# Kernel tuning notes

Measured on AMD Instinct MI355X. Metric: run time of the kernel, lower is better.

Reference implementation:

```python
import jax, jax.numpy as jnp
import numpy as np

B, S, E = 2, 1024, 2048
NH = 8          # num attention heads
KVH = 1         # num key/value heads (GQA)
DH = E // NH    # head dim = 256
CAP = 15.0      # gate soft cap
EPS = 1e-6


def setup_inputs() -> dict:
    key = jax.random.key(0)
    ks = jax.random.split(key, 11)
    g = lambda k, shape, sc=0.02: (jax.random.normal(k, shape, jnp.float32) * sc)
    return {
        "x": jax.random.normal(ks[0], (B, S, E), jnp.float32),
        "Wq": g(ks[1], (E, NH * DH)),
        "Wk": g(ks[2], (E, KVH * DH)),
        "Wv": g(ks[3], (E, KVH * DH)),
        "Wog": g(ks[4], (E, E)),
        "Wi": g(ks[5], (E, NH)),
        "bi": g(ks[6], (NH,), 0.1),
        "Wf": g(ks[7], (E, NH)),
        "bf": jnp.ones((NH,), jnp.float32) * 2.0,  # bias forget gate open, as in xLSTM practice
        "gamma": jnp.ones((E,), jnp.float32),       # multihead layernorm weight
        "Wout": g(ks[8], (E, E)),
    }


def _soft_cap(z):
    return CAP * jnp.tanh(z / CAP)


def _repeat_kv(h, n_rep):
    # (B, KVH, S, DH) -> (B, KVH*n_rep, S, DH)
    if n_rep == 1:
        return h
    b, kvh, s, d = h.shape
    return jnp.broadcast_to(h[:, :, None], (b, kvh, n_rep, s, d)).reshape(b, kvh * n_rep, s, d)


def reference(x, Wq, Wk, Wv, Wog, Wi, bi, Wf, bf, gamma, Wout):
    # --- projections ---
    q = (x @ Wq).reshape(B, S, NH, DH).transpose(0, 2, 1, 3)          # (B,NH,S,DH)
    k = (x @ Wk).reshape(B, S, KVH, DH).transpose(0, 2, 1, 3)         # (B,KVH,S,DH)
    v = (x @ Wv).reshape(B, S, KVH, DH).transpose(0, 2, 1, 3)
    k = _repeat_kv(k, NH // KVH)
    v = _repeat_kv(v, NH // KVH)
    o_preact = x @ Wog                                                # (B,S,E)
    i_pre = _soft_cap(x @ Wi + bi).transpose(0, 2, 1)                 # (B,NH,S)
    f_pre = _soft_cap(x @ Wf + bf).transpose(0, 2, 1)                 # (B,NH,S)

    # --- parallel (stabilized) mLSTM backend ---
    logf = jax.nn.log_sigmoid(f_pre)
    cf = jnp.cumsum(logf, axis=-1)                                    # (B,NH,S)
    mat_logf = cf[:, :, :, None] - cf[:, :, None, :]                  # (B,NH,S,S)
    ltr = jnp.tril(jnp.ones((S, S), dtype=bool))
    mat_logD = jnp.where(ltr, mat_logf, -jnp.inf) + i_pre[:, :, None, :]
    vecM = jnp.max(mat_logD, axis=-1, keepdims=True)                  # (B,NH,S,1)
    matD = jnp.exp(mat_logD - vecM)
    matS = jnp.einsum('bhsd,bhtd->bhst', q, k) * (DH ** -0.5)
    matCt = matS * matD
    vecN = jnp.maximum(jnp.abs(matCt.sum(-1, keepdims=True)), jnp.exp(-vecM))
    matC = matCt / (vecN + EPS)
    h = jnp.einsum('bhst,bhtd->bhsd', matC, v)                        # (B,NH,S,DH)

    # --- multihead layernorm (per-head, float32 reductions) ---
    h = h.transpose(0, 2, 1, 3)                                       # (B,S,NH,DH)
    hf = h.astype(jnp.float32)
    mu = hf.mean(-1, keepdims=True)
    var = hf.var(-1, keepdims=True)
    h_norm = ((hf - mu) * jax.lax.rsqrt(var + EPS)).astype(h.dtype)
    h_norm = (h_norm * gamma.reshape(NH, DH)).reshape(B, S, E)

    # --- output gate + projection ---
    y = (jax.nn.sigmoid(o_preact) * h_norm) @ Wout
    return y
```

## Files before the change

### kernel.cpp

```cpp
#include <hip/hip_runtime.h>
#include <math.h>

#define S_LEN  1024
#define EMB    2048
#define NH_    8
#define DH_    256
#define TOKENS 2048
#define NBH    16
#define NQKVO  4736

typedef __attribute__((ext_vector_type(4))) float    f32x4;
typedef __attribute__((ext_vector_type(8))) _Float16 f16x8;
typedef __attribute__((ext_vector_type(4))) _Float16 f16x4;

__device__ __forceinline__ _Float16 f2h(float f) { return (_Float16)f; }

__device__ __forceinline__ void gload16(const void* g, void* l) {
  __builtin_amdgcn_global_load_lds(
      (const __attribute__((address_space(1))) void*)g,
      (__attribute__((address_space(3))) void*)l, 16, 0, 0);
}

__global__ __launch_bounds__(256) void prep_kernel(
    const float* __restrict__ x,
    const float* __restrict__ Wq, const float* __restrict__ Wk,
    const float* __restrict__ Wv, const float* __restrict__ Wog,
    const float* __restrict__ Wout,
    const float* __restrict__ Wi, const float* __restrict__ Wf,
    _Float16* __restrict__ xh,
    _Float16* __restrict__ WcatT, _Float16* __restrict__ WoutT)
{
  __shared__ float shmem[64][65];
  int t = blockIdx.x;
  const int tid = threadIdx.x;
  if (t < TOKENS) {
    const long base = (long)t * EMB + tid * 8;
    const float4 a = *(const float4*)(x + base);
    const float4 b = *(const float4*)(x + base + 4);
    f16x8 o = {f2h(a.x), f2h(a.y), f2h(a.z), f2h(a.w),
               f2h(b.x), f2h(b.y), f2h(b.z), f2h(b.w)};
    *(f16x8*)(xh + base) = o;
  } else if (t < TOKENS + 3328) {
    t -= TOKENS;
    const float* in; _Float16* out; int ldi, ct;
    if (t < 1024)      { in = Wq;   out = WcatT;                    ldi = 2048; ct = 32; }
    else if (t < 1152) { t -= 1024; in = Wk;  out = WcatT + (long)2048 * EMB; ldi = 256; ct = 4; }
    else if (t < 1280) { t -= 1152; in = Wv;  out = WcatT + (long)2304 * EMB; ldi = 256; ct = 4; }
    else if (t < 2304) { t -= 1280; in = Wog; out = WcatT + (long)2560 * EMB; ldi = 2048; ct = 32; }
    else               { t -= 2304; in = Wout; out = WoutT;         ldi = 2048; ct = 32; }
    const long c0 = (long)(t % ct) * 64, r0 = (long)(t / ct) * 64;
    const int lx = tid & 63, ly = tid >> 6;
    #pragma unroll
    for (int i = 0; i < 16; ++i)
      shmem[ly + i * 4][lx] = in[(r0 + ly + i * 4) * ldi + c0 + lx];
    __syncthreads();
    #pragma unroll
    for (int i = 0; i < 16; ++i)
      out[(c0 + ly + i * 4) * EMB + r0 + lx] = f2h(shmem[lx][ly + i * 4]);
  } else {
    const int j = t - (TOKENS + 3328);
    const int row = 4608 + j * 2 + (tid >> 7);
    const int c0 = (tid & 127) * 16;
    _Float16* dst = WcatT + (long)row * EMB + c0;
    if (row < 4616) {
      const int jj = row - 4608;
      #pragma unroll
      for (int k = 0; k < 16; ++k) dst[k] = f2h(Wi[(long)(c0 + k) * 8 + jj]);
    } else if (row < 4624) {
      const int jj = row - 4616;
      #pragma unroll
      for (int k = 0; k < 16; ++k) dst[k] = f2h(Wf[(long)(c0 + k) * 8 + jj]);
    } else {
      #pragma unroll
      for (int k = 0; k < 16; ++k) dst[k] = (_Float16)0.0f;
    }
  }
}

template<typename CT, int BM>
__global__ __launch_bounds__(256) void gemm_bt_kernel(
    const _Float16* __restrict__ Ag, const _Float16* __restrict__ Btg,
    CT* __restrict__ Cg, int K, int lda, int ldb, int ldc, int mtiles)
{
  constexpr int MR = BM / 32;
  __shared__ _Float16 As[3][BM * 32];
  __shared__ _Float16 Bs[3][128 * 32];
  const int tid = threadIdx.x;
  const int lane = tid & 63, wid = tid >> 6;
  const int cpx = gridDim.x >> 3;
  const int wg = ((int)blockIdx.x & 7) * cpx + ((int)blockIdx.x >> 3);
  const int m0 = (wg % mtiles) * BM;
  const int n0 = (wg / mtiles) * 128;
  const _Float16* Ap = Ag + (long)m0 * lda;
  const _Float16* Bp = Btg + (long)n0 * ldb;
  const int wr = wid >> 1, wc = wid & 1;
  const int lrow = lane & 15, kseg = lane >> 4;

  auto stage = [&](int b, int k0) {
    #pragma unroll
    for (int i = 0; i < BM / 64; ++i) {
      const int cbase = (i * 4 + wid) * 64;
      const int row = (cbase >> 2) + (lane >> 2);
      const int src = ((lane & 3) ^ ((row >> 1) & 3)) * 8;
      gload16(Ap + (long)row * lda + k0 + src, (char*)As[b] + cbase * 16);
    }
    #pragma unroll
    for (int i = 0; i < 2; ++i) {
      const int cbase = (i * 4 + wid) * 64;
      const int row = (cbase >> 2) + (lane >> 2);
      const int src = ((lane & 3) ^ ((row >> 1) & 3)) * 8;
      gload16(Bp + (long)row * ldb + k0 + src, (char*)Bs[b] + cbase * 16);
    }
  };

  const int nt = K >> 5;
  f32x4 acc[MR][4] = {};
  stage(0, 0);
  if (nt > 1) stage(1, 32);
  for (int t = 0; t < nt; ++t) {
    if (t + 2 < nt) {
      stage((t + 2) % 3, (t + 2) * 32);
      if constexpr (BM == 128) asm volatile("s_waitcnt vmcnt(8)" ::: "memory");
      else                     asm volatile("s_waitcnt vmcnt(6)" ::: "memory");
    } else if (t + 1 < nt) {
      if constexpr (BM == 128) asm volatile("s_waitcnt vmcnt(4)" ::: "memory");
      else                     asm volatile("s_waitcnt vmcnt(3)" ::: "memory");
    } else {
      asm volatile("s_waitcnt vmcnt(0)" ::: "memory");
    }
    __builtin_amdgcn_s_barrier();
    __builtin_amdgcn_sched_barrier(0);
    const int buf = t % 3;
    f16x8 fa[MR], fb[4];
    #pragma unroll
    for (int m = 0; m < MR; ++m) {
      const int row = wr * (BM / 2) + m * 16 + lrow;
      fa[m] = *(const f16x8*)&As[buf][row * 32 + ((kseg ^ ((row >> 1) & 3)) << 3)];
    }
    #pragma unroll
    for (int n = 0; n < 4; ++n) {
      const int row = wc * 64 + n * 16 + lrow;
      fb[n] = *(const f16x8*)&Bs[buf][row * 32 + ((kseg ^ ((row >> 1) & 3)) << 3)];
    }
    #pragma unroll
    for (int m = 0; m < MR; ++m)
      #pragma unroll
      for (int n = 0; n < 4; ++n)
        acc[m][n] = __builtin_amdgcn_mfma_f32_16x16x32_f16(fa[m], fb[n], acc[m][n], 0, 0, 0);
    __builtin_amdgcn_s_barrier();
  }
  #pragma unroll
  for (int m = 0; m < MR; ++m)
    #pragma unroll
    for (int n = 0; n < 4; ++n)
      #pragma unroll
      for (int i = 0; i < 4; ++i) {
        const int r = m0 + wr * (BM / 2) + m * 16 + kseg * 4 + i;
        const int c = n0 + wc * 64 + n * 16 + lrow;
        Cg[(long)r * ldc + c] = (CT)acc[m][n][i];
      }
}

__global__ __launch_bounds__(256) void gemm_out_kernel(
    const _Float16* __restrict__ Ag, const _Float16* __restrict__ Btg,
    float* __restrict__ Cg, int K, int lda, int ldb, int ldc, int mtiles)
{
  __shared__ _Float16 As[2][64 * 64];
  __shared__ _Float16 Bs[2][128 * 64];
  const int tid = threadIdx.x;
  const int lane = tid & 63, wid = tid >> 6;
  const int cpx = gridDim.x >> 3;
  const int wg = ((int)blockIdx.x & 7) * cpx + ((int)blockIdx.x >> 3);
  const int m0 = (wg % mtiles) * 64;
  const int n0 = (wg / mtiles) * 128;
  const _Float16* Ap = Ag + (long)m0 * lda;
  const _Float16* Bp = Btg + (long)n0 * ldb;
  const int wr = wid >> 1, wc = wid & 1;
  const int lrow = lane & 15, kseg = lane >> 4;

  auto stage = [&](int b, int k0) {
    #pragma unroll
    for (int i = 0; i < 2; ++i) {
      const int cbase = (i * 4 + wid) * 64;
      const int c = cbase + lane;
      const int row = c >> 3, slot = c & 7;
      gload16(Ap + (long)row * lda + k0 + (slot ^ (row & 7)) * 8,
              (char*)As[b] + cbase * 16);
    }
    #pragma unroll
    for (int i = 0; i < 4; ++i) {
      const int cbase = (i * 4 + wid) * 64;
      const int c = cbase + lane;
      const int row = c >> 3, slot = c & 7;
      gload16(Bp + (long)row * ldb + k0 + (slot ^ (row & 7)) * 8,
              (char*)Bs[b] + cbase * 16);
    }
  };

  const int nt = K >> 6;
  f32x4 acc[2][4] = {};
  stage(0, 0);
  int buf = 0;
  for (int t = 0; t < nt; ++t) {
    if (t + 1 < nt) {
      stage(buf ^ 1, (t + 1) * 64);
      asm volatile("s_waitcnt vmcnt(6)" ::: "memory");
    } else {
      asm volatile("s_waitcnt vmcnt(0)" ::: "memory");
    }
    __builtin_amdgcn_s_barrier();
    __builtin_amdgcn_sched_barrier(0);
    #pragma unroll
    for (int kk = 0; kk < 2; ++kk) {
      f16x8 fa[2], fb[4];
      #pragma unroll
      for (int m = 0; m < 2; ++m) {
        const int row = wr * 32 + m * 16 + lrow;
        fa[m] = *(const f16x8*)&As[buf][row * 64 + (((kk * 4 + kseg) ^ (row & 7)) << 3)];
      }
      #pragma unroll
      for (int n = 0; n < 4; ++n) {
        const int row = wc * 64 + n * 16 + lrow;
        fb[n] = *(const f16x8*)&Bs[buf][row * 64 + (((kk * 4 + kseg) ^ (row & 7)) << 3)];
      }
      #pragma unroll
      for (int m = 0; m < 2; ++m)
        #pragma unroll
        for (int n = 0; n < 4; ++n)
          acc[m][n] = __builtin_amdgcn_mfma_f32_16x16x32_f16(fa[m], fb[n], acc[m][n], 0, 0, 0);
    }
    __builtin_amdgcn_s_barrier();
    buf ^= 1;
  }
  #pragma unroll
  for (int m = 0; m < 2; ++m)
    #pragma unroll
    for (int n = 0; n < 4; ++n)
      #pragma unroll
      for (int i = 0; i < 4; ++i) {
        const int r = m0 + wr * 32 + m * 16 + kseg * 4 + i;
        const int c = n0 + wc * 64 + n * 16 + lrow;
        Cg[(long)r * ldc + c] = acc[m][n][i];
      }
}

__global__ __launch_bounds__(256) void mid_kernel(
    const _Float16* __restrict__ qkvo, _Float16* __restrict__ vt,
    const float* __restrict__ bi, const float* __restrict__ bfg,
    float* __restrict__ aArr, float* __restrict__ mArr, float* __restrict__ vMArr)
{
  __shared__ float shmem[64][65];
  const int tid = threadIdx.x;
  int t = blockIdx.x;
  if (t < NBH) {
    const int bh = t;
    const int b = bh >> 3, h = bh & 7;
    const int lane = tid & 63, wid = tid >> 6;
    float* wsum = &shmem[0][0];
    float* wmax = &shmem[1][0];
    const float bih = bi[h], bfh = bfg[h];
    const int s4 = tid * 4;
    const _Float16* zb = qkvo + (long)(b * S_LEN + s4) * NQKVO;
    float zf[4], zi[4];
    #pragma unroll
    for (int k = 0; k < 4; ++k) {
      zi[k] = 15.0f * tanhf(((float)zb[(long)k * NQKVO + 4608 + h] + bih) * (1.0f / 15.0f));
      zf[k] = 15.0f * tanhf(((float)zb[(long)k * NQKVO + 4616 + h] + bfh) * (1.0f / 15.0f));
    }
    float lg[4];
    #pragma unroll
    for (int k = 0; k < 4; ++k)
      lg[k] = fminf(zf[k], 0.0f) - log1pf(expf(-fabsf(zf[k])));
    float c0 = lg[0], c1 = c0 + lg[1], c2 = c1 + lg[2], c3 = c2 + lg[3];
    float ts = c3;
    #pragma unroll
    for (int off = 1; off < 64; off <<= 1) {
      const float o = __shfl_up(ts, off);
      if (lane >= off) ts += o;
    }
    const float texcl = ts - c3;
    if (lane == 63) wsum[wid] = ts;
    __syncthreads();
    float woff = 0.0f;
    for (int w = 0; w < wid; ++w) woff += wsum[w];
    const float base = woff + texcl;
    const float cf[4] = { base + c0, base + c1, base + c2, base + c3 };
    const float a[4] = { zi[0] - cf[0], zi[1] - cf[1], zi[2] - cf[2], zi[3] - cf[3] };
    float l1 = fmaxf(a[0], a[1]), l3 = fmaxf(fmaxf(l1, a[2]), a[3]);
    float incl = l3;
    #pragma unroll
    for (int off = 1; off < 64; off <<= 1) {
      const float o = __shfl_up(incl, off);
      if (lane >= off) incl = fmaxf(incl, o);
    }
    float excl = __shfl_up(incl, 1);
    if (lane == 0) excl = -3.0e38f;
    if (lane == 63) wmax[wid] = incl;
    __syncthreads();
    float wpre = -3.0e38f;
    for (int w = 0; w < wid; ++w) wpre = fmaxf(wpre, wmax[w]);
    const float pre = fmaxf(wpre, excl);
    float mm[4];
    mm[0] = fmaxf(pre, a[0]); mm[1] = fmaxf(mm[0], a[1]);
    mm[2] = fmaxf(mm[1], a[2]); mm[3] = fmaxf(mm[2], a[3]);
    float4 av = { a[0], a[1], a[2], a[3] };
    float4 mv = { mm[0], mm[1], mm[2], mm[3] };
    float4 vv = { cf[0] + mm[0], cf[1] + mm[1], cf[2] + mm[2], cf[3] + mm[3] };
    *(float4*)(aArr + (long)bh * S_LEN + s4) = av;
    *(float4*)(mArr + (long)bh * S_LEN + s4) = mv;
    *(float4*)(vMArr + (long)bh * S_LEN + s4) = vv;
  } else {
    t -= NBH;
    const int z = t >> 6, rem = t & 63;
    const long c0 = (long)(rem & 3) * 64;
    const long r0 = (long)(rem >> 2) * 64;
    const _Float16* ipt = qkvo + (long)z * S_LEN * NQKVO + 2304;
    _Float16* op = vt + (long)z * DH_ * S_LEN;
    const int lx = tid & 63, ly = tid >> 6;
    #pragma unroll
    for (int i = 0; i < 16; ++i)
      shmem[ly + i * 4][lx] = (float)ipt[(r0 + ly + i * 4) * NQKVO + c0 + lx];
    __syncthreads();
    #pragma unroll
    for (int i = 0; i < 16; ++i)
      op[(c0 + ly + i * 4) * S_LEN + r0 + lx] = f2h(shmem[lx][ly + i * 4]);
  }
}

__global__ __launch_bounds__(512) void att_fused_kernel(
    const _Float16* __restrict__ qkvo, const _Float16* __restrict__ vt,
    const float* __restrict__ aArr, const float* __restrict__ mArr,
    const float* __restrict__ vMArr, const float* __restrict__ gamma,
    _Float16* __restrict__ ub)
{
  __shared__ _Float16 Qs[2][32 * 256];
  __shared__ _Float16 Ws[2][32 * 128];
  __shared__ float nsh[2][8][32];
  __shared__ float s2sh[2][8][32];
  __shared__ float invs[2][32];
  __shared__ float musl[2][32], rssl[2][32];
  const int tid = threadIdx.x;
  const int lane = tid & 63, wid = tid >> 6;
  const int bh = blockIdx.y;
  const int b = bh >> 3, h = bh & 7;
  const int r0[2] = { (int)blockIdx.x * 32, (31 - (int)blockIdx.x) * 32 };
  const _Float16* Qg = qkvo + (long)(b * S_LEN) * NQKVO + h * DH_;
  const _Float16* Kg = qkvo + (long)(b * S_LEN) * NQKVO + 2048;
  const _Float16* Og = qkvo + (long)(b * S_LEN) * NQKVO + 2560 + h * DH_;
  const _Float16* Vt = vt + (long)b * DH_ * S_LEN;
  const float* aA = aArr + (long)bh * S_LEN;
  const float* mA = mArr + (long)bh * S_LEN;
  const float* gam = gamma + h * DH_;
  const int lrow = lane & 15, kseg = lane >> 4;
  const int tbase = 16 * wid;
  const int dbase = 32 * wid;

  #pragma unroll
  for (int i = 0; i < 4; ++i) {
    const int cbase = (i * 8 + wid) * 64;
    const int c = cbase + lane;
    const int sub = c >> 10, row = (c >> 5) & 31, slot = c & 31;
    gload16(Qg + (long)(r0[sub] + row) * NQKVO + (slot ^ (row & 7)) * 8,
            (char*)Qs + cbase * 16);
  }

  float m_s[2][2][4];
  #pragma unroll
  for (int sub = 0; sub < 2; ++sub)
    #pragma unroll
    for (int m = 0; m < 2; ++m)
      #pragma unroll
      for (int i = 0; i < 4; ++i)
        m_s[sub][m][i] = mA[r0[sub] + m * 16 + kseg * 4 + i];
  __syncthreads();

  f32x4 hacc[2][2][2] = {};
  float nacc[2][2][4] = {};
  for (int n0 = 0; n0 <= r0[1]; n0 += 128) {
    f32x4 acc[2][2] = {};
    f16x8 fb, fbn;
    fb = *(const f16x8*)(Kg + (long)(n0 + tbase + lrow) * NQKVO + kseg * 8);
    #pragma unroll
    for (int k0 = 0; k0 < DH_; k0 += 32) {
      if (k0 + 32 < DH_)
        fbn = *(const f16x8*)(Kg + (long)(n0 + tbase + lrow) * NQKVO + k0 + 32 + kseg * 8);
      const int chunk = (k0 >> 3) + kseg;
      __builtin_amdgcn_s_setprio(1);
      #pragma unroll
      for (int sub = 0; sub < 2; ++sub) {
        if (n0 > r0[sub]) continue;
        #pragma unroll
        for (int m = 0; m < 2; ++m) {
          const int qrow = m * 16 + lrow;
          const f16x8 fa = *(const f16x8*)&Qs[sub][qrow * 256 + ((chunk ^ (qrow & 7)) << 3)];
          acc[sub][m] = __builtin_amdgcn_mfma_f32_16x16x32_f16(fa, fb, acc[sub][m], 0, 0, 0);
        }
      }
      __builtin_amdgcn_s_setprio(0);
      fb = fbn;
    }
    const float a_t = aA[n0 + tbase + lrow];
    #pragma unroll
    for (int sub = 0; sub < 2; ++sub) {
      if (n0 > r0[sub]) continue;
      #pragma unroll
      for (int m = 0; m < 2; ++m)
        #pragma unroll
        for (int i = 0; i < 4; ++i) {
          const int sr = m * 16 + kseg * 4 + i;
          const int t  = tbase + lrow;
          float w = 0.0f;
          if (n0 + t <= r0[sub] + sr)
            w = acc[sub][m][i] * 0.0625f * expf(a_t - m_s[sub][m][i]);
          nacc[sub][m][i] += w;
          Ws[sub][sr * 128 + (((t >> 3) ^ ((sr & 7) << 1)) << 3) + (t & 7)] = f2h(w);
        }
    }
    f16x8 vb[2], vbn[2];
    #pragma unroll
    for (int n = 0; n < 2; ++n)
      vb[n] = *(const f16x8*)(Vt + (long)(dbase + n * 16 + lrow) * S_LEN + n0 + kseg * 8);
    __syncthreads();
    #pragma unroll
    for (int kt = 0; kt < 128; kt += 32) {
      if (kt + 32 < 128) {
        #pragma unroll
        for (int n = 0; n < 2; ++n)
          vbn[n] = *(const f16x8*)(Vt + (long)(dbase + n * 16 + lrow) * S_LEN + n0 + kt + 32 + kseg * 8);
      }
      const int chunk = (kt >> 3) + kseg;
      __builtin_amdgcn_s_setprio(1);
      #pragma unroll
      for (int sub = 0; sub < 2; ++sub) {
        if (n0 > r0[sub]) continue;
        #pragma unroll
        for (int m = 0; m < 2; ++m) {
          const int row = m * 16 + lrow;
          const f16x8 wa = *(const f16x8*)&Ws[sub][row * 128 + ((chunk ^ ((row & 7) << 1)) << 3)];
          #pragma unroll
          for (int n = 0; n < 2; ++n)
            hacc[sub][m][n] = __builtin_amdgcn_mfma_f32_16x16x32_f16(wa, vb[n], hacc[sub][m][n], 0, 0, 0);
        }
      }
      __builtin_amdgcn_s_setprio(0);
      vb[0] = vbn[0]; vb[1] = vbn[1];
    }
    __syncthreads();
  }
  #pragma unroll
  for (int sub = 0; sub < 2; ++sub)
    #pragma unroll
    for (int m = 0; m < 2; ++m)
      #pragma unroll
      for (int i = 0; i < 4; ++i) {
        float v = nacc[sub][m][i];
        v += __shfl_xor(v, 1); v += __shfl_xor(v, 2);
        v += __shfl_xor(v, 4); v += __shfl_xor(v, 8);
        if (lrow == 0) nsh[sub][wid][m * 16 + kseg * 4 + i] = v;
      }
  __syncthreads();
  if (tid < 64) {
    const int sub = tid >> 5, sr = tid & 31;
    float tot = 0.0f;
    #pragma unroll
    for (int w = 0; w < 8; ++w) tot += nsh[sub][w][sr];
    const float vm = vMArr[(long)bh * S_LEN + r0[sub] + sr];
    const float vecN = fmaxf(fabsf(tot), expf(-vm));
    invs[sub][sr] = 1.0f / (vecN + 1e-6f);
  }
  __syncthreads();
  #pragma unroll
  for (int sub = 0; sub < 2; ++sub)
    #pragma unroll
    for (int m = 0; m < 2; ++m)
      #pragma unroll
      for (int i = 0; i < 4; ++i) {
        const int row = m * 16 + kseg * 4 + i;
        const float inv = invs[sub][row];
        hacc[sub][m][0][i] *= inv;
        hacc[sub][m][1][i] *= inv;
        float s1 = hacc[sub][m][0][i] + hacc[sub][m][1][i];
        float s2 = hacc[sub][m][0][i] * hacc[sub][m][0][i]
                 + hacc[sub][m][1][i] * hacc[sub][m][1][i];
        s1 += __shfl_xor(s1, 1); s2 += __shfl_xor(s2, 1);
        s1 += __shfl_xor(s1, 2); s2 += __shfl_xor(s2, 2);
        s1 += __shfl_xor(s1, 4); s2 += __shfl_xor(s2, 4);
        s1 += __shfl_xor(s1, 8); s2 += __shfl_xor(s2, 8);
        if (lrow == 0) { nsh[sub][wid][row] = s1; s2sh[sub][wid][row] = s2; }
      }
  __syncthreads();
  if (tid < 64) {
    const int sub = tid >> 5, sr = tid & 31;
    float s1 = 0.0f, s2 = 0.0f;
    #pragma unroll
    for (int w = 0; w < 8; ++w) { s1 += nsh[sub][w][sr]; s2 += s2sh[sub][w][sr]; }
    const float mu = s1 * (1.0f / 256.0f);
    const float var = s2 * (1.0f / 256.0f) - mu * mu;
    musl[sub][sr] = mu;
    rssl[sub][sr] = rsqrtf(var + 1e-6f);
  }
  __syncthreads();
  #pragma unroll
  for (int sub = 0; sub < 2; ++sub)
    #pragma unroll
    for (int m = 0; m < 2; ++m)
      #pragma unroll
      for (int n = 0; n < 2; ++n)
        #pragma unroll
        for (int i = 0; i < 4; ++i) {
          const int row = m * 16 + kseg * 4 + i;
          const int d = dbase + n * 16 + lrow;
          const long gr = r0[sub] + row;
          const float hn = (hacc[sub][m][n][i] - musl[sub][row]) * rssl[sub][row] * gam[d];
          const float o = (float)Og[((long)gr) * NQKVO + d];
          ub[(long)(b * S_LEN + gr) * EMB + h * DH_ + d] =
              f2h(hn * (1.0f / (1.0f + expf(-o))));
        }
}

extern "C" void kernel_launch(void* const* d_in, const int* in_sizes, int n_in,
                              void* d_out, int out_size, void* d_ws, size_t ws_size,
                              hipStream_t stream)
{
  (void)in_sizes; (void)n_in; (void)out_size; (void)ws_size;
  const float* x     = (const float*)d_in[0];
  const float* Wq    = (const float*)d_in[1];
  const float* Wk    = (const float*)d_in[2];
  const float* Wv    = (const float*)d_in[3];
  const float* Wog   = (const float*)d_in[4];
  const float* Wi    = (const float*)d_in[5];
  const float* bi    = (const float*)d_in[6];
  const float* Wf    = (const float*)d_in[7];
  const float* bfg   = (const float*)d_in[8];
  const float* gamma = (const float*)d_in[9];
  const float* Wout  = (const float*)d_in[10];

  char* base = (char*)d_ws;
  size_t off = 0;
  auto take = [&](size_t bytes) -> char* {
    char* p = base + off;
    off += (bytes + 255) & ~(size_t)255;
    return p;
  };
  _Float16* xh    = (_Float16*)take((size_t)TOKENS * EMB * 2);
  _Float16* WcatT = (_Float16*)take((size_t)NQKVO * EMB * 2);
  _Float16* WoutT = (_Float16*)take((size_t)EMB * EMB * 2);
  _Float16* qkvo  = (_Float16*)take((size_t)TOKENS * NQKVO * 2);
  _Float16* vt    = (_Float16*)take((size_t)2 * DH_ * S_LEN * 2);
  _Float16* ub    = (_Float16*)take((size_t)TOKENS * EMB * 2);
  float*    aA    = (float*)take((size_t)NBH * S_LEN * 4);
  float*    mA    = (float*)take((size_t)NBH * S_LEN * 4);
  float*    vM    = (float*)take((size_t)NBH * S_LEN * 4);
  float*    y     = (float*)d_out;

  const dim3 blk(256);
  prep_kernel<<<dim3(TOKENS + 3328 + 64), blk, 0, stream>>>(
      x, Wq, Wk, Wv, Wog, Wout, Wi, Wf, xh, WcatT, WoutT);
  gemm_bt_kernel<_Float16, 128><<<dim3(16 * 37), blk, 0, stream>>>(
      xh, WcatT, qkvo, EMB, EMB, EMB, NQKVO, 16);
  mid_kernel<<<dim3(NBH + 128), blk, 0, stream>>>(qkvo, vt, bi, bfg, aA, mA, vM);
  att_fused_kernel<<<dim3(16, NBH), dim3(512), 0, stream>>>(
      qkvo, vt, aA, mA, vM, gamma, ub);
  gemm_out_kernel<<<dim3(32 * 16), blk, 0, stream>>>(
      ub, WoutT, y, EMB, EMB, EMB, EMB, 32);
}
```

Measured before the change: 159.4 us.

## Restructure QKVO projection GEMM to 512-thread blocks with BK=64 double buffering

```diff
diff --git a/kernel.cpp b/kernel.cpp
--- a/kernel.cpp
+++ b/kernel.cpp
@@ -77,87 +77,86 @@
   }
 }
 
-template<typename CT, int BM>
-__global__ __launch_bounds__(256) void gemm_bt_kernel(
+__global__ __launch_bounds__(512, 4) void gemm_qkvo_kernel(
     const _Float16* __restrict__ Ag, const _Float16* __restrict__ Btg,
-    CT* __restrict__ Cg, int K, int lda, int ldb, int ldc, int mtiles)
+    _Float16* __restrict__ Cg, int K, int lda, int ldb, int ldc, int mtiles)
 {
-  constexpr int MR = BM / 32;
-  __shared__ _Float16 As[3][BM * 32];
-  __shared__ _Float16 Bs[3][128 * 32];
+  __shared__ _Float16 As[2][128 * 64];
+  __shared__ _Float16 Bs[2][128 * 64];
   const int tid = threadIdx.x;
   const int lane = tid & 63, wid = tid >> 6;
   const int cpx = gridDim.x >> 3;
   const int wg = ((int)blockIdx.x & 7) * cpx + ((int)blockIdx.x >> 3);
-  const int m0 = (wg % mtiles) * BM;
+  const int m0 = (wg % mtiles) * 128;
   const int n0 = (wg / mtiles) * 128;
   const _Float16* Ap = Ag + (long)m0 * lda;
   const _Float16* Bp = Btg + (long)n0 * ldb;
-  const int wr = wid >> 1, wc = wid & 1;
+  const int wr = wid >> 2, wc = wid & 3;
   const int lrow = lane & 15, kseg = lane >> 4;
 
   auto stage = [&](int b, int k0) {
     #pragma unroll
-    for (int i = 0; i < BM / 64; ++i) {
-      const int cbase = (i * 4 + wid) * 64;
-      const int row = (cbase >> 2) + (lane >> 2);
-      const int src = ((lane & 3) ^ ((row >> 1) & 3)) * 8;
-      gload16(Ap + (long)row * lda + k0 + src, (char*)As[b] + cbase * 16);
-    }
-    #pragma unroll
     for (int i = 0; i < 2; ++i) {
-      const int cbase = (i * 4 + wid) * 64;
-      const int row = (cbase >> 2) + (lane >> 2);
-      const int src = ((lane & 3) ^ ((row >> 1) & 3)) * 8;
-      gload16(Bp + (long)row * ldb + k0 + src, (char*)Bs[b] + cbase * 16);
+      const int cbase = (i * 8 + wid) * 64;
+      const int c = cbase + lane;
+      const int row = c >> 3, slot = c & 7;
+      gload16(Ap + (long)row * lda + k0 + (slot ^ (row & 7)) * 8,
+              (char*)As[b] + cbase * 16);
+    }
+    #pragma unroll
+    for (int i = 0; i < 2; ++i) {
+      const int cbase = (i * 8 + wid) * 64;
+      const int c = cbase + lane;
+      const int row = c >> 3, slot = c & 7;
+      gload16(Bp + (long)row * ldb + k0 + (slot ^ (row & 7)) * 8,
+              (char*)Bs[b] + cbase * 16);
     }
   };
 
-  const int nt = K >> 5;
-  f32x4 acc[MR][4] = {};
+  const int nt = K >> 6;
+  f32x4 acc[4][2] = {};
   stage(0, 0);
-  if (nt > 1) stage(1, 32);
+  int buf = 0;
   for (int t = 0; t < nt; ++t) {
-    if (t + 2 < nt) {
-      stage((t + 2) % 3, (t + 2) * 32);
-      if constexpr (BM == 128) asm volatile("s_waitcnt vmcnt(8)" ::: "memory");
-      else                     asm volatile("s_waitcnt vmcnt(6)" ::: "memory");
-    } else if (t + 1 < nt) {
-      if constexpr (BM == 128) asm volatile("s_waitcnt vmcnt(4)" ::: "memory");
-      else                     asm volatile("s_waitcnt vmcnt(3)" ::: "memory");
+    if (t + 1 < nt) {
+      stage(buf ^ 1, (t + 1) * 64);
+      asm volatile("s_waitcnt vmcnt(4)" ::: "memory");
     } else {
       asm volatile("s_waitcnt vmcnt(0)" ::: "memory");
     }
     __builtin_amdgcn_s_barrier();
     __builtin_amdgcn_sched_barrier(0);
-    const int buf = t % 3;
-    f16x8 fa[MR], fb[4];
-    #pragma unroll
-    for (int m = 0; m < MR; ++m) {
-      const int row = wr * (BM / 2) + m * 16 + lrow;
-      fa[m] = *(const f16x8*)&As[buf][row * 32 + ((kseg ^ ((row >> 1) & 3)) << 3)];
-    }
-    #pragma unroll
-    for (int n = 0; n < 4; ++n) {
-      const int row = wc * 64 + n * 16 + lrow;
-      fb[n] = *(const f16x8*)&Bs[buf][row * 32 + ((kseg ^ ((row >> 1) & 3)) << 3)];
-    }
-    #pragma unroll
-    for (int m = 0; m < MR; ++m)
-      #pragma unroll
-      for (int n = 0; n < 4; ++n)
-        acc[m][n] = __builtin_amdgcn_mfma_f32_16x16x32_f16(fa[m], fb[n], acc[m][n], 0, 0, 0);
+    #pragma unroll
+    for (int kk = 0; kk < 2; ++kk) {
+      f16x8 fa[4], fb[2];
+      #pragma unroll
+      for (int m = 0; m < 4; ++m) {
+        const int row = wr * 64 + m * 16 + lrow;
+        fa[m] = *(const f16x8*)&As[buf][row * 64 + (((kk * 4 + kseg) ^ (row & 7)) << 3)];
+      }
+      #pragma unroll
+      for (int n = 0; n < 2; ++n) {
+        const int row = wc * 32 + n * 16 + lrow;
+        fb[n] = *(const f16x8*)&Bs[buf][row * 64 + (((kk * 4 + kseg) ^ (row & 7)) << 3)];
+      }
+      #pragma unroll
+      for (int m = 0; m < 4; ++m)
+        #pragma unroll
+        for (int n = 0; n < 2; ++n)
+          acc[m][n] = __builtin_amdgcn_mfma_f32_16x16x32_f16(fa[m], fb[n], acc[m][n], 0, 0, 0);
+    }
     __builtin_amdgcn_s_barrier();
-  }
-  #pragma unroll
-  for (int m = 0; m < MR; ++m)
-    #pragma unroll
-    for (int n = 0; n < 4; ++n)
+    buf ^= 1;
+  }
+  #pragma unroll
+  for (int m = 0; m < 4; ++m)
+    #pragma unroll
+    for (int n = 0; n < 2; ++n)
       #pragma unroll
       for (int i = 0; i < 4; ++i) {
-        const int r = m0 + wr * (BM / 2) + m * 16 + kseg * 4 + i;
-        const int c = n0 + wc * 64 + n * 16 + lrow;
-        Cg[(long)r * ldc + c] = (CT)acc[m][n][i];
+        const int r = m0 + wr * 64 + m * 16 + kseg * 4 + i;
+        const int c = n0 + wc * 32 + n * 16 + lrow;
+        Cg[(long)r * ldc + c] = (_Float16)acc[m][n][i];
       }
 }
 
@@ -556,7 +555,7 @@
   const dim3 blk(256);
   prep_kernel<<<dim3(TOKENS + 3328 + 64), blk, 0, stream>>>(
       x, Wq, Wk, Wv, Wog, Wout, Wi, Wf, xh, WcatT, WoutT);
-  gemm_bt_kernel<_Float16, 128><<<dim3(16 * 37), blk, 0, stream>>>(
+  gemm_qkvo_kernel<<<dim3(16 * 37), dim3(512), 0, stream>>>(
       xh, WcatT, qkvo, EMB, EMB, EMB, NQKVO, 16);
   mid_kernel<<<dim3(NBH + 128), blk, 0, stream>>>(qkvo, vt, bi, bfg, aA, mA, vM);
   att_fused_kernel<<<dim3(16, NBH), dim3(512), 0, stream>>>(
```

Result: slower. 170.5 us (+6.9%).
